# Performance work log

Hardware: AMD Instinct MI355X
Metric: run time of the kernel (lower is better)

The kernel has to match this reference:

```python
import jax, jax.numpy as jnp
import numpy as np

B, NB, S, D = 4096, 16, 256, 1024


def setup_inputs() -> dict:
    key = jax.random.key(0)
    k = jax.random.split(key, 6)
    sc_in = 1.0 / np.sqrt(D)
    sc_out = 1.0 / np.sqrt(S)
    return {
        "x": jax.random.normal(k[0], (B, D), dtype=jnp.float32),
        "y_index": jax.random.randint(k[1], (B, 1), 0, NB, dtype=jnp.int64),
        "W_in": jax.random.uniform(k[2], (NB, S, D), jnp.float32, -sc_in, sc_in),
        "b_in": jax.random.uniform(k[3], (NB, S), jnp.float32, -sc_in, sc_in),
        "W_out": jax.random.uniform(k[4], (NB, D, S), jnp.float32, -sc_out, sc_out),
        "b_out": jax.random.uniform(k[5], (NB, D), jnp.float32, -sc_out, sc_out),
    }


def reference(x, y_index, W_in, b_in, W_out, b_out):
    # h: [B, D] -> relu applied before every branch's fc_in (as in torch source)
    h = jax.nn.relu(x)
    # hiddens for all branches: [B, NB, S]
    hid = jnp.einsum("bd,nsd->bns", h, W_in) + b_in[None, :, :]
    # branch outputs stacked: [B, NB, D]
    outs = jnp.einsum("bns,nds->bnd", hid, W_out) + b_out[None, :, :]
    # gather selected branch per token: [B, D]
    sel = jnp.take_along_axis(outs, y_index[:, :, None], axis=1)[:, 0, :]
    return x + sel
```

## Files before the change

### kernel.cpp

```cpp
#include <hip/hip_runtime.h>


typedef unsigned short u16;
typedef short bf16x8 __attribute__((ext_vector_type(8)));
typedef float f32x4 __attribute__((ext_vector_type(4)));

#define MFMA16 __builtin_amdgcn_mfma_f32_16x16x32_bf16

constexpr int B_TOK = 4096;
constexpr int NB = 16;
constexpr int S_DIM = 256;
constexpr int D_DIM = 1024;
constexpr int BM = 64;
constexpr int PAD_ROWS = B_TOK + NB * BM;
constexpr int NTILES = PAD_ROWS / BM;
constexpr int W_ITEMS = NB * S_DIM * D_DIM / 8;

__device__ __forceinline__ unsigned short f2bf(float f) {
    unsigned u = __builtin_bit_cast(unsigned, f);
    u += 0x7fffu + ((u >> 16) & 1u);
    return (unsigned short)(u >> 16);
}
__device__ __forceinline__ unsigned pack2(float a, float b) {
    return (unsigned)f2bf(a) | ((unsigned)f2bf(b) << 16);
}
__device__ __forceinline__ void gload_lds16(const void* g, void* l) {
    __builtin_amdgcn_global_load_lds(
        (const __attribute__((address_space(1))) void*)g,
        (__attribute__((address_space(3))) void*)l, 16, 0, 0);
}
__device__ __forceinline__ void publish() {
    asm volatile("s_waitcnt vmcnt(0)" ::: "memory");
    __syncthreads();
}
__device__ __forceinline__ void cast8(const float* __restrict__ src,
                                      u16* __restrict__ dst, int j) {
    const float4* p = (const float4*)src + (size_t)j * 2;
    float4 v0 = p[0], v1 = p[1];
    uint4 o;
    o.x = pack2(v0.x, v0.y);
    o.y = pack2(v0.z, v0.w);
    o.z = pack2(v1.x, v1.y);
    o.w = pack2(v1.z, v1.w);
    ((uint4*)dst)[j] = o;
}

__global__ __launch_bounds__(256) void prep_kernel(
    const float* __restrict__ Wi_f, u16* __restrict__ Wi,
    const int* __restrict__ y, int* __restrict__ perm, int* __restrict__ tileBranch) {
    const int t = threadIdx.x;
    if (blockIdx.x == 0) {
        __shared__ int hist[NB];
        __shared__ int aoff[NB + 1];
        __shared__ int cursor[NB];
        if (t < NB) hist[t] = 0;
        __syncthreads();
        for (int i = t; i < B_TOK; i += 256) atomicAdd(&hist[y[i]], 1);
        __syncthreads();
        if (t == 0) {
            int off = 0;
            for (int n = 0; n < NB; ++n) {
                aoff[n] = off;
                cursor[n] = off;
                off += ((hist[n] + BM - 1) / BM) * BM;
            }
            aoff[NB] = off;
        }
        __syncthreads();
        for (int i = t; i < NTILES; i += 256) {
            int rb = i * BM, br = -1;
            for (int n = 0; n < NB; ++n)
                if (rb >= aoff[n] && rb < aoff[n + 1]) br = n;
            tileBranch[i] = br;
        }
        for (int i = t; i < PAD_ROWS; i += 256) perm[i] = -1;
        __syncthreads();
        for (int i = t; i < B_TOK; i += 256) {
            int pos = atomicAdd(&cursor[y[i]], 1);
            perm[pos] = i;
        }
        return;
    }
    cast8(Wi_f, Wi, (blockIdx.x - 1) * 256 + t);
}

__global__ __launch_bounds__(256) void gemm1_kernel(
    const float* __restrict__ x, const u16* __restrict__ Wi,
    const float* __restrict__ b_in, const int* __restrict__ tileBranch,
    const int* __restrict__ perm, u16* __restrict__ Hp,
    const float* __restrict__ Wo_f, u16* __restrict__ Wo) {
    const int branch = tileBranch[blockIdx.y];
    const int t = threadIdx.x;

    if (branch >= 0) {
        const int rowBase = blockIdx.y * BM;
        const int colBase = blockIdx.x * 64;

        __shared__ u16 sA[2][64 * 64];
        __shared__ u16 sB[2][64 * 64];

        const int sr = t >> 2;
        const int scg = t & 3;
        const int tok = perm[rowBase + sr];
        const float* aSrc = (tok >= 0) ? (x + (size_t)tok * D_DIM + scg * 16) : x;
        const int sbyte0 = (sr * 128 + scg * 32) ^ ((sr & 7) << 4);
        const int sbyte1 = sbyte0 ^ 16;

        const u16* Bb = Wi + (size_t)branch * S_DIM * D_DIM + (size_t)colBase * D_DIM;

        const int lane = t & 63;
        const int wid = t >> 6;
        const int wm = (wid >> 1) * 32;
        const int wn = (wid & 1) * 32;
        const int fr = lane & 15;
        const int kc = (lane >> 4) << 3;

        f32x4 acc[2][2] = {};
        float4 av0, av1, av2, av3;

        auto loadA = [&](int k0) {
            const float4* pa = (const float4*)(aSrc + k0);
            av0 = pa[0]; av1 = pa[1]; av2 = pa[2]; av3 = pa[3];
        };
        auto stageB = [&](int buf, int k0) {
#pragma unroll
            for (int i = 0; i < 2; ++i) {
                const int L = i * 4096 + t * 16;
                const int row = L >> 7;
                const int sunit = ((L >> 4) & 7) ^ (row & 7);
                gload_lds16((const char*)Bb + (size_t)row * (D_DIM * 2) + k0 * 2 + sunit * 16,
                            (char*)sB[buf] + L);
            }
        };
        auto packWriteA = [&](int buf) {
            uint4 w0, w1;
            if (tok >= 0) {
                w0.x = pack2(fmaxf(av0.x, 0.f), fmaxf(av0.y, 0.f));
                w0.y = pack2(fmaxf(av0.z, 0.f), fmaxf(av0.w, 0.f));
                w0.z = pack2(fmaxf(av1.x, 0.f), fmaxf(av1.y, 0.f));
                w0.w = pack2(fmaxf(av1.z, 0.f), fmaxf(av1.w, 0.f));
                w1.x = pack2(fmaxf(av2.x, 0.f), fmaxf(av2.y, 0.f));
                w1.y = pack2(fmaxf(av2.z, 0.f), fmaxf(av2.w, 0.f));
                w1.z = pack2(fmaxf(av3.x, 0.f), fmaxf(av3.y, 0.f));
                w1.w = pack2(fmaxf(av3.z, 0.f), fmaxf(av3.w, 0.f));
            } else {
                w0 = make_uint4(0, 0, 0, 0);
                w1 = make_uint4(0, 0, 0, 0);
            }
            *(uint4*)((char*)sA[buf] + sbyte0) = w0;
            *(uint4*)((char*)sA[buf] + sbyte1) = w1;
        };

        loadA(0);
        stageB(0, 0);
        packWriteA(0);
        publish();

        for (int kt = 0; kt < 16; ++kt) {
            const int cur = kt & 1;
            if (kt < 15) {
                stageB(cur ^ 1, (kt + 1) << 6);
                loadA((kt + 1) << 6);
            }
#pragma unroll
            for (int kk = 0; kk < 2; ++kk) {
                const int kcol = kc + kk * 32;
                const int ra0 = wm + fr, ra1 = wm + 16 + fr;
                const int rb0 = wn + fr, rb1 = wn + 16 + fr;
                bf16x8 a0 = *(const bf16x8*)&sA[cur][(ra0 * 64 + kcol) ^ ((ra0 & 7) << 3)];
                bf16x8 a1 = *(const bf16x8*)&sA[cur][(ra1 * 64 + kcol) ^ ((ra1 & 7) << 3)];
                bf16x8 b0 = *(const bf16x8*)&sB[cur][(rb0 * 64 + kcol) ^ ((rb0 & 7) << 3)];
                bf16x8 b1 = *(const bf16x8*)&sB[cur][(rb1 * 64 + kcol) ^ ((rb1 & 7) << 3)];
                acc[0][0] = MFMA16(a0, b0, acc[0][0], 0, 0, 0);
                acc[0][1] = MFMA16(a0, b1, acc[0][1], 0, 0, 0);
                acc[1][0] = MFMA16(a1, b0, acc[1][0], 0, 0, 0);
                acc[1][1] = MFMA16(a1, b1, acc[1][1], 0, 0, 0);
            }
            if (kt < 15) packWriteA(cur ^ 1);
            publish();
        }

        const int r0 = (lane >> 4) * 4;
#pragma unroll
        for (int m = 0; m < 2; ++m) {
            const int prow0 = rowBase + wm + m * 16 + r0;
#pragma unroll
            for (int n = 0; n < 2; ++n) {
                const int col = colBase + wn + n * 16 + fr;
                const float bvs = b_in[branch * S_DIM + col];
#pragma unroll
                for (int r = 0; r < 4; ++r)
                    Hp[(size_t)(prow0 + r) * S_DIM + col] = f2bf(acc[m][n][r] + bvs);
            }
        }
    }

    const int bid = blockIdx.y * 4 + blockIdx.x;
    for (int j = bid * 256 + t; j < W_ITEMS; j += 4 * NTILES * 256)
        cast8(Wo_f, Wo, j);
}

__global__ __launch_bounds__(256) void gemm2_kernel(
    const u16* __restrict__ Hp, const u16* __restrict__ Wo,
    const float* __restrict__ b_out, const int* __restrict__ tileBranch,
    const int* __restrict__ perm, const float* __restrict__ x,
    float* __restrict__ out) {
    const int branch = tileBranch[blockIdx.y];
    if (branch < 0) return;
    const int rowBase = blockIdx.y * BM;
    const int colBase = blockIdx.x * 128;

    __shared__ __align__(16) char smem[49152];
    u16* sA0 = (u16*)smem;
    u16* sA1 = (u16*)(smem + 8192);
    u16* sB0 = (u16*)(smem + 16384);
    u16* sB1 = (u16*)(smem + 32768);

    const int t = threadIdx.x;
    const u16* Ab = Hp + (size_t)rowBase * S_DIM;
    const u16* Bb = Wo + (size_t)branch * D_DIM * S_DIM + (size_t)colBase * S_DIM;

    const int lane = t & 63;
    const int wid = t >> 6;
    const int wm = (wid >> 1) * 32;
    const int wn = (wid & 1) * 64;
    const int fr = lane & 15;
    const int kc = (lane >> 4) << 3;

    f32x4 acc[2][4] = {};

    auto stage = [&](u16* dA, u16* dB, int k0) {
#pragma unroll
        for (int i = 0; i < 2; ++i) {
            const int L = i * 4096 + t * 16;
            const int row = L >> 7;
            const int sunit = ((L >> 4) & 7) ^ (row & 7);
            gload_lds16((const char*)Ab + (size_t)row * (S_DIM * 2) + k0 * 2 + sunit * 16,
                        (char*)dA + L);
        }
#pragma unroll
        for (int i = 0; i < 4; ++i) {
            const int L = i * 4096 + t * 16;
            const int row = L >> 7;
            const int sunit = ((L >> 4) & 7) ^ (row & 7);
            gload_lds16((const char*)Bb + (size_t)row * (S_DIM * 2) + k0 * 2 + sunit * 16,
                        (char*)dB + L);
        }
    };
    auto compute = [&](const u16* cA, const u16* cB) {
#pragma unroll
        for (int kk = 0; kk < 2; ++kk) {
            const int kcol = kc + kk * 32;
            const int ra0 = wm + fr, ra1 = wm + 16 + fr;
            bf16x8 a0 = *(const bf16x8*)&cA[(ra0 * 64 + kcol) ^ ((ra0 & 7) << 3)];
            bf16x8 a1 = *(const bf16x8*)&cA[(ra1 * 64 + kcol) ^ ((ra1 & 7) << 3)];
            bf16x8 b[4];
#pragma unroll
            for (int n = 0; n < 4; ++n) {
                const int rb = wn + n * 16 + fr;
                b[n] = *(const bf16x8*)&cB[(rb * 64 + kcol) ^ ((rb & 7) << 3)];
            }
#pragma unroll
            for (int n = 0; n < 4; ++n) {
                acc[0][n] = MFMA16(a0, b[n], acc[0][n], 0, 0, 0);
                acc[1][n] = MFMA16(a1, b[n], acc[1][n], 0, 0, 0);
            }
        }
    };

    stage(sA0, sB0, 0);
    publish();
#pragma unroll
    for (int kt = 0; kt < 4; ++kt) {
        const bool even = (kt & 1) == 0;
        u16* cA = even ? sA0 : sA1;
        u16* cB = even ? sB0 : sB1;
        u16* nA = even ? sA1 : sA0;
        u16* nB = even ? sB1 : sB0;
        if (kt < 3) stage(nA, nB, (kt + 1) << 6);
        compute(cA, cB);
        publish();
    }

    float* bo = (float*)smem;
    const int r0 = (lane >> 4) * 4;
#pragma unroll
    for (int m = 0; m < 2; ++m)
#pragma unroll
        for (int n = 0; n < 4; ++n)
#pragma unroll
            for (int r = 0; r < 4; ++r)
                bo[(wm + m * 16 + r0 + r) * 132 + wn + n * 16 + fr] = acc[m][n][r];
    __syncthreads();

    const int erow = t >> 2;
    const int q4 = (t & 3) * 4;
    const int tok2 = perm[rowBase + erow];
    if (tok2 >= 0) {
        const size_t gbase = (size_t)tok2 * D_DIM + colBase;
        const float* xr = x + gbase;
        float* orow = out + gbase;
        const float* br = b_out + (size_t)branch * D_DIM + colBase;
#pragma unroll
        for (int j = 0; j < 8; ++j) {
            const int c = q4 + j * 16;
            float4 xv = *(const float4*)&xr[c];
            float4 bvv = *(const float4*)&br[c];
            float4 hv = *(const float4*)&bo[erow * 132 + c];
            float4 s;
            s.x = xv.x + bvv.x + hv.x;
            s.y = xv.y + bvv.y + hv.y;
            s.z = xv.z + bvv.z + hv.z;
            s.w = xv.w + bvv.w + hv.w;
            *(float4*)&orow[c] = s;
        }
    }
}

extern "C" void kernel_launch(void* const* d_in, const int* in_sizes, int n_in,
                              void* d_out, int out_size, void* d_ws, size_t ws_size,
                              hipStream_t stream) {
    const float* x     = (const float*)d_in[0];
    const int*   y     = (const int*)d_in[1];
    const float* W_in  = (const float*)d_in[2];
    const float* b_in  = (const float*)d_in[3];
    const float* W_out = (const float*)d_in[4];
    const float* b_out = (const float*)d_in[5];
    float* out = (float*)d_out;

    char* ws = (char*)d_ws;
    u16* Wi = (u16*)(ws);
    u16* Wo = (u16*)(ws + 8388608);
    u16* Hp = (u16*)(ws + 16777216);
    int* perm = (int*)(ws + 19398656);
    int* tileBranch = (int*)(ws + 19419136);

    prep_kernel<<<2049, 256, 0, stream>>>(W_in, Wi, y, perm, tileBranch);

    gemm1_kernel<<<dim3(S_DIM / 64, NTILES), 256, 0, stream>>>(
        x, Wi, b_in, tileBranch, perm, Hp, W_out, Wo);

    gemm2_kernel<<<dim3(D_DIM / 128, NTILES), 256, 0, stream>>>(
        Hp, Wo, b_out, tileBranch, perm, x, out);
}
```

Before: 56.21 us.

## Split-K gemm1 with reduce kernel, move W_out cast to prep, narrow gemm2 tiles

gemm1 is now split along K into four z-slices. Each slice writes fp32 partial sums, and a new reduce kernel adds them, applies b_in and packs the result to bf16. This raises the block count for the small first GEMM. The W_out bf16 cast moves from the tail of gemm1 into prep_kernel. gemm2 tiles shrink from 128 to 64 columns to double its grid. The cost is an extra launch plus the write and read of about 20MB of fp32 partials.

Result: no change. 55.35 us (-1.5%).

```diff
diff --git a/kernel.cpp b/kernel.cpp
--- a/kernel.cpp
+++ b/kernel.cpp
@@ -14,7 +14,8 @@
 constexpr int BM = 64;
 constexpr int PAD_ROWS = B_TOK + NB * BM;
 constexpr int NTILES = PAD_ROWS / BM;
-constexpr int W_ITEMS = NB * S_DIM * D_DIM / 8;
+constexpr int KSPLIT = 4;
+constexpr int HP_ELEMS = PAD_ROWS * S_DIM;
 
 __device__ __forceinline__ unsigned short f2bf(float f) {
     unsigned u = __builtin_bit_cast(unsigned, f);
@@ -46,7 +47,8 @@
 }
 
 __global__ __launch_bounds__(256) void prep_kernel(
-    const float* __restrict__ Wi_f, u16* __restrict__ Wi,
+    const float* __restrict__ Wi_f, const float* __restrict__ Wo_f,
+    u16* __restrict__ Wi, u16* __restrict__ Wo,
     const int* __restrict__ y, int* __restrict__ perm, int* __restrict__ tileBranch) {
     const int t = threadIdx.x;
     if (blockIdx.x == 0) {
@@ -81,123 +83,150 @@
         }
         return;
     }
-    cast8(Wi_f, Wi, (blockIdx.x - 1) * 256 + t);
+    int i = (blockIdx.x - 1) * 256 + t;
+    if (i < 524288) cast8(Wi_f, Wi, i);
+    else            cast8(Wo_f, Wo, i - 524288);
 }
 
 __global__ __launch_bounds__(256) void gemm1_kernel(
     const float* __restrict__ x, const u16* __restrict__ Wi,
-    const float* __restrict__ b_in, const int* __restrict__ tileBranch,
-    const int* __restrict__ perm, u16* __restrict__ Hp,
-    const float* __restrict__ Wo_f, u16* __restrict__ Wo) {
+    const int* __restrict__ tileBranch, const int* __restrict__ perm,
+    float* __restrict__ Hpart) {
     const int branch = tileBranch[blockIdx.y];
+    if (branch < 0) return;
+    const int rowBase = blockIdx.y * BM;
+    const int colBase = blockIdx.x * 64;
+    const int kbase = blockIdx.z * (D_DIM / KSPLIT);
+
+    __shared__ u16 sA[2][64 * 64];
+    __shared__ u16 sB[2][64 * 64];
+
     const int t = threadIdx.x;
-
-    if (branch >= 0) {
-        const int rowBase = blockIdx.y * BM;
-        const int colBase = blockIdx.x * 64;
-
-        __shared__ u16 sA[2][64 * 64];
-        __shared__ u16 sB[2][64 * 64];
-
-        const int sr = t >> 2;
-        const int scg = t & 3;
-        const int tok = perm[rowBase + sr];
-        const float* aSrc = (tok >= 0) ? (x + (size_t)tok * D_DIM + scg * 16) : x;
-        const int sbyte0 = (sr * 128 + scg * 32) ^ ((sr & 7) << 4);
-        const int sbyte1 = sbyte0 ^ 16;
-
-        const u16* Bb = Wi + (size_t)branch * S_DIM * D_DIM + (size_t)colBase * D_DIM;
-
-        const int lane = t & 63;
-        const int wid = t >> 6;
-        const int wm = (wid >> 1) * 32;
-        const int wn = (wid & 1) * 32;
-        const int fr = lane & 15;
-        const int kc = (lane >> 4) << 3;
-
-        f32x4 acc[2][2] = {};
-        float4 av0, av1, av2, av3;
-
-        auto loadA = [&](int k0) {
-            const float4* pa = (const float4*)(aSrc + k0);
-            av0 = pa[0]; av1 = pa[1]; av2 = pa[2]; av3 = pa[3];
-        };
-        auto stageB = [&](int buf, int k0) {
-#pragma unroll
-            for (int i = 0; i < 2; ++i) {
-                const int L = i * 4096 + t * 16;
-                const int row = L >> 7;
-                const int sunit = ((L >> 4) & 7) ^ (row & 7);
-                gload_lds16((const char*)Bb + (size_t)row * (D_DIM * 2) + k0 * 2 + sunit * 16,
-                            (char*)sB[buf] + L);
-            }
-        };
-        auto packWriteA = [&](int buf) {
-            uint4 w0, w1;
-            if (tok >= 0) {
-                w0.x = pack2(fmaxf(av0.x, 0.f), fmaxf(av0.y, 0.f));
-                w0.y = pack2(fmaxf(av0.z, 0.f), fmaxf(av0.w, 0.f));
-                w0.z = pack2(fmaxf(av1.x, 0.f), fmaxf(av1.y, 0.f));
-                w0.w = pack2(fmaxf(av1.z, 0.f), fmaxf(av1.w, 0.f));
-                w1.x = pack2(fmaxf(av2.x, 0.f), fmaxf(av2.y, 0.f));
-                w1.y = pack2(fmaxf(av2.z, 0.f), fmaxf(av2.w, 0.f));
-                w1.z = pack2(fmaxf(av3.x, 0.f), fmaxf(av3.y, 0.f));
-                w1.w = pack2(fmaxf(av3.z, 0.f), fmaxf(av3.w, 0.f));
-            } else {
-                w0 = make_uint4(0, 0, 0, 0);
-                w1 = make_uint4(0, 0, 0, 0);
-            }
-            *(uint4*)((char*)sA[buf] + sbyte0) = w0;
-            *(uint4*)((char*)sA[buf] + sbyte1) = w1;
-        };
-
-        loadA(0);
-        stageB(0, 0);
-        packWriteA(0);
+    const int sr = t >> 2;
+    const int scg = t & 3;
+    const int tok = perm[rowBase + sr];
+    const float* aSrc = (tok >= 0) ? (x + (size_t)tok * D_DIM + scg * 16) : x;
+    const int sbyte0 = (sr * 128 + scg * 32) ^ ((sr & 7) << 4);
+    const int sbyte1 = sbyte0 ^ 16;
+
+    const u16* Bb = Wi + (size_t)branch * S_DIM * D_DIM + (size_t)colBase * D_DIM;
+
+    const int lane = t & 63;
+    const int wid = t >> 6;
+    const int wm = (wid >> 1) * 32;
+    const int wn = (wid & 1) * 32;
+    const int fr = lane & 15;
+    const int kc = (lane >> 4) << 3;
+
+    f32x4 acc[2][2] = {};
+    float4 av0, av1, av2, av3;
+
+    auto loadA = [&](int k0) {
+        const float4* pa = (const float4*)(aSrc + k0);
+        av0 = pa[0]; av1 = pa[1]; av2 = pa[2]; av3 = pa[3];
+    };
+    auto stageB = [&](int buf, int k0) {
+#pragma unroll
+        for (int i = 0; i < 2; ++i) {
+            const int L = i * 4096 + t * 16;
+            const int row = L >> 7;
+            const int sunit = ((L >> 4) & 7) ^ (row & 7);
+            gload_lds16((const char*)Bb + (size_t)row * (D_DIM * 2) + k0 * 2 + sunit * 16,
+                        (char*)sB[buf] + L);
+        }
+    };
+    auto packWriteA = [&](int buf) {
+        uint4 w0, w1;
+        if (tok >= 0) {
+            w0.x = pack2(fmaxf(av0.x, 0.f), fmaxf(av0.y, 0.f));
+            w0.y = pack2(fmaxf(av0.z, 0.f), fmaxf(av0.w, 0.f));
+            w0.z = pack2(fmaxf(av1.x, 0.f), fmaxf(av1.y, 0.f));
+            w0.w = pack2(fmaxf(av1.z, 0.f), fmaxf(av1.w, 0.f));
+            w1.x = pack2(fmaxf(av2.x, 0.f), fmaxf(av2.y, 0.f));
+            w1.y = pack2(fmaxf(av2.z, 0.f), fmaxf(av2.w, 0.f));
+            w1.z = pack2(fmaxf(av3.x, 0.f), fmaxf(av3.y, 0.f));
+            w1.w = pack2(fmaxf(av3.z, 0.f), fmaxf(av3.w, 0.f));
+        } else {
+            w0 = make_uint4(0, 0, 0, 0);
+            w1 = make_uint4(0, 0, 0, 0);
+        }
+        *(uint4*)((char*)sA[buf] + sbyte0) = w0;
+        *(uint4*)((char*)sA[buf] + sbyte1) = w1;
+    };
+
+    loadA(kbase);
+    stageB(0, kbase);
+    packWriteA(0);
+    publish();
+
+    for (int kt = 0; kt < 4; ++kt) {
+        const int cur = kt & 1;
+        if (kt < 3) {
+            const int k0n = kbase + ((kt + 1) << 6);
+            stageB(cur ^ 1, k0n);
+            loadA(k0n);
+        }
+#pragma unroll
+        for (int kk = 0; kk < 2; ++kk) {
+            const int kcol = kc + kk * 32;
+            const int ra0 = wm + fr, ra1 = wm + 16 + fr;
+            const int rb0 = wn + fr, rb1 = wn + 16 + fr;
+            bf16x8 a0 = *(const bf16x8*)&sA[cur][(ra0 * 64 + kcol) ^ ((ra0 & 7) << 3)];
+            bf16x8 a1 = *(const bf16x8*)&sA[cur][(ra1 * 64 + kcol) ^ ((ra1 & 7) << 3)];
+            bf16x8 b0 = *(const bf16x8*)&sB[cur][(rb0 * 64 + kcol) ^ ((rb0 & 7) << 3)];
+            bf16x8 b1 = *(const bf16x8*)&sB[cur][(rb1 * 64 + kcol) ^ ((rb1 & 7) << 3)];
+            acc[0][0] = MFMA16(a0, b0, acc[0][0], 0, 0, 0);
+            acc[0][1] = MFMA16(a0, b1, acc[0][1], 0, 0, 0);
+            acc[1][0] = MFMA16(a1, b0, acc[1][0], 0, 0, 0);
+            acc[1][1] = MFMA16(a1, b1, acc[1][1], 0, 0, 0);
+        }
+        if (kt < 3) packWriteA(cur ^ 1);
         publish();
-
-        for (int kt = 0; kt < 16; ++kt) {
-            const int cur = kt & 1;
-            if (kt < 15) {
-                stageB(cur ^ 1, (kt + 1) << 6);
-                loadA((kt + 1) << 6);
-            }
-#pragma unroll
-            for (int kk = 0; kk < 2; ++kk) {
-                const int kcol = kc + kk * 32;
-                const int ra0 = wm + fr, ra1 = wm + 16 + fr;
-                const int rb0 = wn + fr, rb1 = wn + 16 + fr;
-                bf16x8 a0 = *(const bf16x8*)&sA[cur][(ra0 * 64 + kcol) ^ ((ra0 & 7) << 3)];
-                bf16x8 a1 = *(const bf16x8*)&sA[cur][(ra1 * 64 + kcol) ^ ((ra1 & 7) << 3)];
-                bf16x8 b0 = *(const bf16x8*)&sB[cur][(rb0 * 64 + kcol) ^ ((rb0 & 7) << 3)];
-                bf16x8 b1 = *(const bf16x8*)&sB[cur][(rb1 * 64 + kcol) ^ ((rb1 & 7) << 3)];
-                acc[0][0] = MFMA16(a0, b0, acc[0][0], 0, 0, 0);
-                acc[0][1] = MFMA16(a0, b1, acc[0][1], 0, 0, 0);
-                acc[1][0] = MFMA16(a1, b0, acc[1][0], 0, 0, 0);
-                acc[1][1] = MFMA16(a1, b1, acc[1][1], 0, 0, 0);
-            }
-            if (kt < 15) packWriteA(cur ^ 1);
-            publish();
-        }
-
-        const int r0 = (lane >> 4) * 4;
-#pragma unroll
-        for (int m = 0; m < 2; ++m) {
-            const int prow0 = rowBase + wm + m * 16 + r0;
-#pragma unroll
-            for (int n = 0; n < 2; ++n) {
-                const int col = colBase + wn + n * 16 + fr;
-                const float bvs = b_in[branch * S_DIM + col];
-#pragma unroll
-                for (int r = 0; r < 4; ++r)
-                    Hp[(size_t)(prow0 + r) * S_DIM + col] = f2bf(acc[m][n][r] + bvs);
-            }
-        }
-    }
-
-    const int bid = blockIdx.y * 4 + blockIdx.x;
-    for (int j = bid * 256 + t; j < W_ITEMS; j += 4 * NTILES * 256)
-        cast8(Wo_f, Wo, j);
+    }
+
+    float* Op = Hpart + (size_t)blockIdx.z * HP_ELEMS;
+    const int r0 = (lane >> 4) * 4;
+#pragma unroll
+    for (int m = 0; m < 2; ++m) {
+        const int prow0 = rowBase + wm + m * 16 + r0;
+#pragma unroll
+        for (int n = 0; n < 2; ++n) {
+            const int col = colBase + wn + n * 16 + fr;
+#pragma unroll
+            for (int r = 0; r < 4; ++r)
+                Op[(size_t)(prow0 + r) * S_DIM + col] = acc[m][n][r];
+        }
+    }
+}
+
+__global__ __launch_bounds__(256) void reduce_kernel(
+    const float* __restrict__ Hpart, const float* __restrict__ b_in,
+    const int* __restrict__ tileBranch, u16* __restrict__ Hp) {
+    const int j = blockIdx.x * 256 + threadIdx.x;
+    const int row = j >> 5;
+    const int c8 = (j & 31) << 3;
+    const int branch = tileBranch[row >> 6];
+    if (branch < 0) return;
+    const float* p = Hpart + (size_t)row * S_DIM + c8;
+    float4 s0 = *(const float4*)p;
+    float4 s1 = *(const float4*)(p + 4);
+#pragma unroll
+    for (int ks = 1; ks < KSPLIT; ++ks) {
+        const float* q = p + (size_t)ks * HP_ELEMS;
+        float4 a0 = *(const float4*)q;
+        float4 a1 = *(const float4*)(q + 4);
+        s0.x += a0.x; s0.y += a0.y; s0.z += a0.z; s0.w += a0.w;
+        s1.x += a1.x; s1.y += a1.y; s1.z += a1.z; s1.w += a1.w;
+    }
+    const float* bp = b_in + (size_t)branch * S_DIM + c8;
+    float4 b0 = *(const float4*)bp;
+    float4 b1 = *(const float4*)(bp + 4);
+    uint4 o;
+    o.x = pack2(s0.x + b0.x, s0.y + b0.y);
+    o.y = pack2(s0.z + b0.z, s0.w + b0.w);
+    o.z = pack2(s1.x + b1.x, s1.y + b1.y);
+    o.w = pack2(s1.z + b1.z, s1.w + b1.w);
+    *(uint4*)&Hp[(size_t)row * S_DIM + c8] = o;
 }
 
 __global__ __launch_bounds__(256) void gemm2_kernel(
@@ -208,13 +237,13 @@
     const int branch = tileBranch[blockIdx.y];
     if (branch < 0) return;
     const int rowBase = blockIdx.y * BM;
-    const int colBase = blockIdx.x * 128;
-
-    __shared__ __align__(16) char smem[49152];
+    const int colBase = blockIdx.x * 64;
+
+    __shared__ __align__(16) char smem[32768];
     u16* sA0 = (u16*)smem;
     u16* sA1 = (u16*)(smem + 8192);
     u16* sB0 = (u16*)(smem + 16384);
-    u16* sB1 = (u16*)(smem + 32768);
+    u16* sB1 = (u16*)(smem + 24576);
 
     const int t = threadIdx.x;
     const u16* Ab = Hp + (size_t)rowBase * S_DIM;
@@ -223,11 +252,11 @@
     const int lane = t & 63;
     const int wid = t >> 6;
     const int wm = (wid >> 1) * 32;
-    const int wn = (wid & 1) * 64;
+    const int wn = (wid & 1) * 32;
     const int fr = lane & 15;
     const int kc = (lane >> 4) << 3;
 
-    f32x4 acc[2][4] = {};
+    f32x4 acc[2][2] = {};
 
     auto stage = [&](u16* dA, u16* dB, int k0) {
 #pragma unroll
@@ -239,7 +268,7 @@
                         (char*)dA + L);
         }
 #pragma unroll
-        for (int i = 0; i < 4; ++i) {
+        for (int i = 0; i < 2; ++i) {
             const int L = i * 4096 + t * 16;
             const int row = L >> 7;
             const int sunit = ((L >> 4) & 7) ^ (row & 7);
@@ -252,19 +281,15 @@
         for (int kk = 0; kk < 2; ++kk) {
             const int kcol = kc + kk * 32;
             const int ra0 = wm + fr, ra1 = wm + 16 + fr;
+            const int rb0 = wn + fr, rb1 = wn + 16 + fr;
             bf16x8 a0 = *(const bf16x8*)&cA[(ra0 * 64 + kcol) ^ ((ra0 & 7) << 3)];
             bf16x8 a1 = *(const bf16x8*)&cA[(ra1 * 64 + kcol) ^ ((ra1 & 7) << 3)];
-            bf16x8 b[4];
-#pragma unroll
-            for (int n = 0; n < 4; ++n) {
-                const int rb = wn + n * 16 + fr;
-                b[n] = *(const bf16x8*)&cB[(rb * 64 + kcol) ^ ((rb & 7) << 3)];
-            }
-#pragma unroll
-            for (int n = 0; n < 4; ++n) {
-                acc[0][n] = MFMA16(a0, b[n], acc[0][n], 0, 0, 0);
-                acc[1][n] = MFMA16(a1, b[n], acc[1][n], 0, 0, 0);
-            }
+            bf16x8 b0 = *(const bf16x8*)&cB[(rb0 * 64 + kcol) ^ ((rb0 & 7) << 3)];
+            bf16x8 b1 = *(const bf16x8*)&cB[(rb1 * 64 + kcol) ^ ((rb1 & 7) << 3)];
+            acc[0][0] = MFMA16(a0, b0, acc[0][0], 0, 0, 0);
+            acc[0][1] = MFMA16(a0, b1, acc[0][1], 0, 0, 0);
+            acc[1][0] = MFMA16(a1, b0, acc[1][0], 0, 0, 0);
+            acc[1][1] = MFMA16(a1, b1, acc[1][1], 0, 0, 0);
         }
     };
 
@@ -287,10 +312,10 @@
 #pragma unroll
     for (int m = 0; m < 2; ++m)
 #pragma unroll
-        for (int n = 0; n < 4; ++n)
+        for (int n = 0; n < 2; ++n)
 #pragma unroll
             for (int r = 0; r < 4; ++r)
-                bo[(wm + m * 16 + r0 + r) * 132 + wn + n * 16 + fr] = acc[m][n][r];
+                bo[(wm + m * 16 + r0 + r) * 68 + wn + n * 16 + fr] = acc[m][n][r];
     __syncthreads();
 
     const int erow = t >> 2;
@@ -302,11 +327,11 @@
         float* orow = out + gbase;
         const float* br = b_out + (size_t)branch * D_DIM + colBase;
 #pragma unroll
-        for (int j = 0; j < 8; ++j) {
+        for (int j = 0; j < 4; ++j) {
             const int c = q4 + j * 16;
             float4 xv = *(const float4*)&xr[c];
             float4 bvv = *(const float4*)&br[c];
-            float4 hv = *(const float4*)&bo[erow * 132 + c];
+            float4 hv = *(const float4*)&bo[erow * 68 + c];
             float4 s;
             s.x = xv.x + bvv.x + hv.x;
             s.y = xv.y + bvv.y + hv.y;
@@ -332,14 +357,17 @@
     u16* Wi = (u16*)(ws);
     u16* Wo = (u16*)(ws + 8388608);
     u16* Hp = (u16*)(ws + 16777216);
-    int* perm = (int*)(ws + 19398656);
-    int* tileBranch = (int*)(ws + 19419136);
-
-    prep_kernel<<<2049, 256, 0, stream>>>(W_in, Wi, y, perm, tileBranch);
-
-    gemm1_kernel<<<dim3(S_DIM / 64, NTILES), 256, 0, stream>>>(
-        x, Wi, b_in, tileBranch, perm, Hp, W_out, Wo);
-
-    gemm2_kernel<<<dim3(D_DIM / 128, NTILES), 256, 0, stream>>>(
+    float* Hpart = (float*)(ws + 19398656);
+    int* perm = (int*)(ws + 40370176);
+    int* tileBranch = (int*)(ws + 40390656);
+
+    prep_kernel<<<4097, 256, 0, stream>>>(W_in, W_out, Wi, Wo, y, perm, tileBranch);
+
+    gemm1_kernel<<<dim3(4, NTILES, KSPLIT), 256, 0, stream>>>(
+        x, Wi, tileBranch, perm, Hpart);
+
+    reduce_kernel<<<640, 256, 0, stream>>>(Hpart, b_in, tileBranch, Hp);
+
+    gemm2_kernel<<<dim3(16, NTILES), 256, 0, stream>>>(
         Hp, Wo, b_out, tileBranch, perm, x, out);
 }
```

## Move W_out cast into prep kernel and shrink GEMM tiles for more blocks

Applied to the files above, without the earlier changes.

Casting of W_out to bf16 moves out of gemm1's tail and into the prep kernel, which now converts both weight tensors in one launch. gemm1 now uses 32-row M tiles instead of 64, and gemm2 uses 64-column N tiles instead of 128, so each GEMM launches more blocks and fills the GPU better. The costs are more redundant weight-tile loads per block, less reuse per block, and a longer prep kernel that sits on the critical path before gemm1.

New measurement: 51.22 us. 1.1x faster.

```diff
diff --git a/kernel.cpp b/kernel.cpp
--- a/kernel.cpp
+++ b/kernel.cpp
@@ -14,7 +14,7 @@
 constexpr int BM = 64;
 constexpr int PAD_ROWS = B_TOK + NB * BM;
 constexpr int NTILES = PAD_ROWS / BM;
-constexpr int W_ITEMS = NB * S_DIM * D_DIM / 8;
+constexpr int NTILES32 = PAD_ROWS / 32;
 
 __device__ __forceinline__ unsigned short f2bf(float f) {
     unsigned u = __builtin_bit_cast(unsigned, f);
@@ -46,7 +46,8 @@
 }
 
 __global__ __launch_bounds__(256) void prep_kernel(
-    const float* __restrict__ Wi_f, u16* __restrict__ Wi,
+    const float* __restrict__ Wi_f, const float* __restrict__ Wo_f,
+    u16* __restrict__ Wi, u16* __restrict__ Wo,
     const int* __restrict__ y, int* __restrict__ perm, int* __restrict__ tileBranch) {
     const int t = threadIdx.x;
     if (blockIdx.x == 0) {
@@ -81,123 +82,106 @@
         }
         return;
     }
-    cast8(Wi_f, Wi, (blockIdx.x - 1) * 256 + t);
+    int i = (blockIdx.x - 1) * 256 + t;
+    if (i < 524288) cast8(Wi_f, Wi, i);
+    else            cast8(Wo_f, Wo, i - 524288);
 }
 
 __global__ __launch_bounds__(256) void gemm1_kernel(
     const float* __restrict__ x, const u16* __restrict__ Wi,
     const float* __restrict__ b_in, const int* __restrict__ tileBranch,
-    const int* __restrict__ perm, u16* __restrict__ Hp,
-    const float* __restrict__ Wo_f, u16* __restrict__ Wo) {
-    const int branch = tileBranch[blockIdx.y];
+    const int* __restrict__ perm, u16* __restrict__ Hp) {
+    const int branch = tileBranch[blockIdx.y >> 1];
+    if (branch < 0) return;
+    const int rowBase = blockIdx.y * 32;
+    const int colBase = blockIdx.x * 64;
     const int t = threadIdx.x;
 
-    if (branch >= 0) {
-        const int rowBase = blockIdx.y * BM;
-        const int colBase = blockIdx.x * 64;
-
-        __shared__ u16 sA[2][64 * 64];
-        __shared__ u16 sB[2][64 * 64];
-
-        const int sr = t >> 2;
-        const int scg = t & 3;
-        const int tok = perm[rowBase + sr];
-        const float* aSrc = (tok >= 0) ? (x + (size_t)tok * D_DIM + scg * 16) : x;
-        const int sbyte0 = (sr * 128 + scg * 32) ^ ((sr & 7) << 4);
-        const int sbyte1 = sbyte0 ^ 16;
-
-        const u16* Bb = Wi + (size_t)branch * S_DIM * D_DIM + (size_t)colBase * D_DIM;
-
-        const int lane = t & 63;
-        const int wid = t >> 6;
-        const int wm = (wid >> 1) * 32;
-        const int wn = (wid & 1) * 32;
-        const int fr = lane & 15;
-        const int kc = (lane >> 4) << 3;
-
-        f32x4 acc[2][2] = {};
-        float4 av0, av1, av2, av3;
-
-        auto loadA = [&](int k0) {
-            const float4* pa = (const float4*)(aSrc + k0);
-            av0 = pa[0]; av1 = pa[1]; av2 = pa[2]; av3 = pa[3];
-        };
-        auto stageB = [&](int buf, int k0) {
-#pragma unroll
-            for (int i = 0; i < 2; ++i) {
-                const int L = i * 4096 + t * 16;
-                const int row = L >> 7;
-                const int sunit = ((L >> 4) & 7) ^ (row & 7);
-                gload_lds16((const char*)Bb + (size_t)row * (D_DIM * 2) + k0 * 2 + sunit * 16,
-                            (char*)sB[buf] + L);
-            }
-        };
-        auto packWriteA = [&](int buf) {
-            uint4 w0, w1;
-            if (tok >= 0) {
-                w0.x = pack2(fmaxf(av0.x, 0.f), fmaxf(av0.y, 0.f));
-                w0.y = pack2(fmaxf(av0.z, 0.f), fmaxf(av0.w, 0.f));
-                w0.z = pack2(fmaxf(av1.x, 0.f), fmaxf(av1.y, 0.f));
-                w0.w = pack2(fmaxf(av1.z, 0.f), fmaxf(av1.w, 0.f));
-                w1.x = pack2(fmaxf(av2.x, 0.f), fmaxf(av2.y, 0.f));
-                w1.y = pack2(fmaxf(av2.z, 0.f), fmaxf(av2.w, 0.f));
-                w1.z = pack2(fmaxf(av3.x, 0.f), fmaxf(av3.y, 0.f));
-                w1.w = pack2(fmaxf(av3.z, 0.f), fmaxf(av3.w, 0.f));
-            } else {
-                w0 = make_uint4(0, 0, 0, 0);
-                w1 = make_uint4(0, 0, 0, 0);
-            }
-            *(uint4*)((char*)sA[buf] + sbyte0) = w0;
-            *(uint4*)((char*)sA[buf] + sbyte1) = w1;
-        };
-
-        loadA(0);
-        stageB(0, 0);
-        packWriteA(0);
+    __shared__ u16 sA[2][32 * 64];
+    __shared__ u16 sB[2][64 * 64];
+
+    const int sr = t >> 3;
+    const int scg = t & 7;
+    const int tok = perm[rowBase + sr];
+    const float* aSrc = (tok >= 0) ? (x + (size_t)tok * D_DIM + scg * 8) : x;
+    const int sbyte = (sr * 128 + scg * 16) ^ ((sr & 7) << 4);
+
+    const u16* Bb = Wi + (size_t)branch * S_DIM * D_DIM + (size_t)colBase * D_DIM;
+
+    const int lane = t & 63;
+    const int wid = t >> 6;
+    const int wm = (wid >> 1) * 16;
+    const int wn = (wid & 1) * 32;
+    const int fr = lane & 15;
+    const int kc = (lane >> 4) << 3;
+
+    f32x4 acc[2] = {};
+    float4 av0, av1;
+
+    auto loadA = [&](int k0) {
+        const float4* pa = (const float4*)(aSrc + k0);
+        av0 = pa[0]; av1 = pa[1];
+    };
+    auto stageB = [&](int buf, int k0) {
+#pragma unroll
+        for (int i = 0; i < 2; ++i) {
+            const int L = i * 4096 + t * 16;
+            const int row = L >> 7;
+            const int sunit = ((L >> 4) & 7) ^ (row & 7);
+            gload_lds16((const char*)Bb + (size_t)row * (D_DIM * 2) + k0 * 2 + sunit * 16,
+                        (char*)sB[buf] + L);
+        }
+    };
+    auto packWriteA = [&](int buf) {
+        uint4 w;
+        if (tok >= 0) {
+            w.x = pack2(fmaxf(av0.x, 0.f), fmaxf(av0.y, 0.f));
+            w.y = pack2(fmaxf(av0.z, 0.f), fmaxf(av0.w, 0.f));
+            w.z = pack2(fmaxf(av1.x, 0.f), fmaxf(av1.y, 0.f));
+            w.w = pack2(fmaxf(av1.z, 0.f), fmaxf(av1.w, 0.f));
+        } else {
+            w = make_uint4(0, 0, 0, 0);
+        }
+        *(uint4*)((char*)sA[buf] + sbyte) = w;
+    };
+
+    loadA(0);
+    stageB(0, 0);
+    packWriteA(0);
+    publish();
+
+    for (int kt = 0; kt < 16; ++kt) {
+        const int cur = kt & 1;
+        if (kt < 15) {
+            const int k0n = (kt + 1) << 6;
+            stageB(cur ^ 1, k0n);
+            loadA(k0n);
+        }
+#pragma unroll
+        for (int kk = 0; kk < 2; ++kk) {
+            const int kcol = kc + kk * 32;
+            const int ra = wm + fr;
+            const int rb0 = wn + fr, rb1 = wn + 16 + fr;
+            bf16x8 a0 = *(const bf16x8*)&sA[cur][(ra * 64 + kcol) ^ ((ra & 7) << 3)];
+            bf16x8 b0 = *(const bf16x8*)&sB[cur][(rb0 * 64 + kcol) ^ ((rb0 & 7) << 3)];
+            bf16x8 b1 = *(const bf16x8*)&sB[cur][(rb1 * 64 + kcol) ^ ((rb1 & 7) << 3)];
+            acc[0] = MFMA16(a0, b0, acc[0], 0, 0, 0);
+            acc[1] = MFMA16(a0, b1, acc[1], 0, 0, 0);
+        }
+        if (kt < 15) packWriteA(cur ^ 1);
         publish();
-
-        for (int kt = 0; kt < 16; ++kt) {
-            const int cur = kt & 1;
-            if (kt < 15) {
-                stageB(cur ^ 1, (kt + 1) << 6);
-                loadA((kt + 1) << 6);
-            }
-#pragma unroll
-            for (int kk = 0; kk < 2; ++kk) {
-                const int kcol = kc + kk * 32;
-                const int ra0 = wm + fr, ra1 = wm + 16 + fr;
-                const int rb0 = wn + fr, rb1 = wn + 16 + fr;
-                bf16x8 a0 = *(const bf16x8*)&sA[cur][(ra0 * 64 + kcol) ^ ((ra0 & 7) << 3)];
-                bf16x8 a1 = *(const bf16x8*)&sA[cur][(ra1 * 64 + kcol) ^ ((ra1 & 7) << 3)];
-                bf16x8 b0 = *(const bf16x8*)&sB[cur][(rb0 * 64 + kcol) ^ ((rb0 & 7) << 3)];
-                bf16x8 b1 = *(const bf16x8*)&sB[cur][(rb1 * 64 + kcol) ^ ((rb1 & 7) << 3)];
-                acc[0][0] = MFMA16(a0, b0, acc[0][0], 0, 0, 0);
-                acc[0][1] = MFMA16(a0, b1, acc[0][1], 0, 0, 0);
-                acc[1][0] = MFMA16(a1, b0, acc[1][0], 0, 0, 0);
-                acc[1][1] = MFMA16(a1, b1, acc[1][1], 0, 0, 0);
-            }
-            if (kt < 15) packWriteA(cur ^ 1);
-            publish();
-        }
-
-        const int r0 = (lane >> 4) * 4;
-#pragma unroll
-        for (int m = 0; m < 2; ++m) {
-            const int prow0 = rowBase + wm + m * 16 + r0;
-#pragma unroll
-            for (int n = 0; n < 2; ++n) {
-                const int col = colBase + wn + n * 16 + fr;
-                const float bvs = b_in[branch * S_DIM + col];
-#pragma unroll
-                for (int r = 0; r < 4; ++r)
-                    Hp[(size_t)(prow0 + r) * S_DIM + col] = f2bf(acc[m][n][r] + bvs);
-            }
-        }
-    }
-
-    const int bid = blockIdx.y * 4 + blockIdx.x;
-    for (int j = bid * 256 + t; j < W_ITEMS; j += 4 * NTILES * 256)
-        cast8(Wo_f, Wo, j);
+    }
+
+    const int r0 = (lane >> 4) * 4;
+    const int prow0 = rowBase + wm + r0;
+#pragma unroll
+    for (int n = 0; n < 2; ++n) {
+        const int col = colBase + wn + n * 16 + fr;
+        const float bvs = b_in[branch * S_DIM + col];
+#pragma unroll
+        for (int r = 0; r < 4; ++r)
+            Hp[(size_t)(prow0 + r) * S_DIM + col] = f2bf(acc[n][r] + bvs);
+    }
 }
 
 __global__ __launch_bounds__(256) void gemm2_kernel(
@@ -208,13 +192,13 @@
     const int branch = tileBranch[blockIdx.y];
     if (branch < 0) return;
     const int rowBase = blockIdx.y * BM;
-    const int colBase = blockIdx.x * 128;
-
-    __shared__ __align__(16) char smem[49152];
+    const int colBase = blockIdx.x * 64;
+
+    __shared__ __align__(16) char smem[32768];
     u16* sA0 = (u16*)smem;
     u16* sA1 = (u16*)(smem + 8192);
     u16* sB0 = (u16*)(smem + 16384);
-    u16* sB1 = (u16*)(smem + 32768);
+    u16* sB1 = (u16*)(smem + 24576);
 
     const int t = threadIdx.x;
     const u16* Ab = Hp + (size_t)rowBase * S_DIM;
@@ -223,11 +207,11 @@
     const int lane = t & 63;
     const int wid = t >> 6;
     const int wm = (wid >> 1) * 32;
-    const int wn = (wid & 1) * 64;
+    const int wn = (wid & 1) * 32;
     const int fr = lane & 15;
     const int kc = (lane >> 4) << 3;
 
-    f32x4 acc[2][4] = {};
+    f32x4 acc[2][2] = {};
 
     auto stage = [&](u16* dA, u16* dB, int k0) {
 #pragma unroll
@@ -239,7 +223,7 @@
                         (char*)dA + L);
         }
 #pragma unroll
-        for (int i = 0; i < 4; ++i) {
+        for (int i = 0; i < 2; ++i) {
             const int L = i * 4096 + t * 16;
             const int row = L >> 7;
             const int sunit = ((L >> 4) & 7) ^ (row & 7);
@@ -252,19 +236,15 @@
         for (int kk = 0; kk < 2; ++kk) {
             const int kcol = kc + kk * 32;
             const int ra0 = wm + fr, ra1 = wm + 16 + fr;
+            const int rb0 = wn + fr, rb1 = wn + 16 + fr;
             bf16x8 a0 = *(const bf16x8*)&cA[(ra0 * 64 + kcol) ^ ((ra0 & 7) << 3)];
             bf16x8 a1 = *(const bf16x8*)&cA[(ra1 * 64 + kcol) ^ ((ra1 & 7) << 3)];
-            bf16x8 b[4];
-#pragma unroll
-            for (int n = 0; n < 4; ++n) {
-                const int rb = wn + n * 16 + fr;
-                b[n] = *(const bf16x8*)&cB[(rb * 64 + kcol) ^ ((rb & 7) << 3)];
-            }
-#pragma unroll
-            for (int n = 0; n < 4; ++n) {
-                acc[0][n] = MFMA16(a0, b[n], acc[0][n], 0, 0, 0);
-                acc[1][n] = MFMA16(a1, b[n], acc[1][n], 0, 0, 0);
-            }
+            bf16x8 b0 = *(const bf16x8*)&cB[(rb0 * 64 + kcol) ^ ((rb0 & 7) << 3)];
+            bf16x8 b1 = *(const bf16x8*)&cB[(rb1 * 64 + kcol) ^ ((rb1 & 7) << 3)];
+            acc[0][0] = MFMA16(a0, b0, acc[0][0], 0, 0, 0);
+            acc[0][1] = MFMA16(a0, b1, acc[0][1], 0, 0, 0);
+            acc[1][0] = MFMA16(a1, b0, acc[1][0], 0, 0, 0);
+            acc[1][1] = MFMA16(a1, b1, acc[1][1], 0, 0, 0);
         }
     };
 
@@ -287,10 +267,10 @@
 #pragma unroll
     for (int m = 0; m < 2; ++m)
 #pragma unroll
-        for (int n = 0; n < 4; ++n)
+        for (int n = 0; n < 2; ++n)
 #pragma unroll
             for (int r = 0; r < 4; ++r)
-                bo[(wm + m * 16 + r0 + r) * 132 + wn + n * 16 + fr] = acc[m][n][r];
+                bo[(wm + m * 16 + r0 + r) * 68 + wn + n * 16 + fr] = acc[m][n][r];
     __syncthreads();
 
     const int erow = t >> 2;
@@ -302,11 +282,11 @@
         float* orow = out + gbase;
         const float* br = b_out + (size_t)branch * D_DIM + colBase;
 #pragma unroll
-        for (int j = 0; j < 8; ++j) {
+        for (int j = 0; j < 4; ++j) {
             const int c = q4 + j * 16;
             float4 xv = *(const float4*)&xr[c];
             float4 bvv = *(const float4*)&br[c];
-            float4 hv = *(const float4*)&bo[erow * 132 + c];
+            float4 hv = *(const float4*)&bo[erow * 68 + c];
             float4 s;
             s.x = xv.x + bvv.x + hv.x;
             s.y = xv.y + bvv.y + hv.y;
@@ -335,11 +315,11 @@
     int* perm = (int*)(ws + 19398656);
     int* tileBranch = (int*)(ws + 19419136);
 
-    prep_kernel<<<2049, 256, 0, stream>>>(W_in, Wi, y, perm, tileBranch);
-
-    gemm1_kernel<<<dim3(S_DIM / 64, NTILES), 256, 0, stream>>>(
-        x, Wi, b_in, tileBranch, perm, Hp, W_out, Wo);
-
-    gemm2_kernel<<<dim3(D_DIM / 128, NTILES), 256, 0, stream>>>(
+    prep_kernel<<<4097, 256, 0, stream>>>(W_in, W_out, Wi, Wo, y, perm, tileBranch);
+
+    gemm1_kernel<<<dim3(4, NTILES32), 256, 0, stream>>>(
+        x, Wi, b_in, tileBranch, perm, Hp);
+
+    gemm2_kernel<<<dim3(16, NTILES), 256, 0, stream>>>(
         Hp, Wo, b_out, tileBranch, perm, x, out);
 }
```
